# Kernel tuning notes

Measured on AMD Instinct MI355X. Metric: run time of the kernel, lower is better.

The kernel has to match this reference:

```python
import jax, jax.numpy as jnp
import numpy as np
from jax import lax

HEADS = 8
DIM_HEAD = 8
SCALE = DIM_HEAD ** (-0.5)
UP = 64  # nn.Upsample(scale_factor=64), nearest


def _conv_s8(x, w, b):
    # Conv2d(inner, inner, 11x11, stride 8, padding 2) + exact GELU
    y = lax.conv_general_dilated(x, w, window_strides=(8, 8),
                                 padding=((2, 2), (2, 2)),
                                 dimension_numbers=('NCHW', 'OIHW', 'NCHW'))
    return jax.nn.gelu(y + b[None, :, None, None], approximate=False)


def setup_inputs() -> dict:
    key = jax.random.key(0)
    ks = jax.random.split(key, 8)
    b, c, h, w = 2, 64, 48, 48
    inner = HEADS * DIM_HEAD  # 64
    f = jax.random.normal(ks[0], (b, c, h, w), jnp.float32)
    w_qkv = jax.random.normal(ks[1], (inner * 3, c, 1, 1), jnp.float32) * 0.05
    wq = jax.random.normal(ks[2], (inner, inner, 11, 11), jnp.float32) * 0.02
    bq = jax.random.normal(ks[3], (inner,), jnp.float32) * 0.02
    wk = jax.random.normal(ks[4], (inner, inner, 11, 11), jnp.float32) * 0.02
    bk = jax.random.normal(ks[5], (inner,), jnp.float32) * 0.02
    pos_h = jax.random.normal(ks[6], (DIM_HEAD, h), jnp.float32) * SCALE
    pos_w = jax.random.normal(ks[7], (DIM_HEAD, w), jnp.float32) * SCALE
    return {"f": f, "w_qkv": w_qkv, "wq": wq, "bq": bq, "wk": wk,
            "bk": bk, "pos_h": pos_h, "pos_w": pos_w}


def reference(f, w_qkv, wq, bq, wk, bk, pos_h, pos_w):
    b, c, h, w = f.shape
    inner = HEADS * DIM_HEAD
    # 1x1 conv to qkv
    qkv = jnp.einsum('oc,bchw->bohw', w_qkv[:, :, 0, 0], f)
    q, k, v = jnp.split(qkv, 3, axis=1)  # each [b, inner, h, w]
    # positional logits from pre-conv q
    q_full = q.reshape(b, HEADS, DIM_HEAD, h * w)
    emb = (pos_h[:, :, None] + pos_w[:, None, :]).reshape(DIM_HEAD, h * w)
    pos_logits = jnp.einsum('bhci,cj->bhij', q_full, emb)  # [b,H,hw,hw]
    # strided conv + gelu on q,k
    qd = _conv_s8(q, wq, bq)
    kd = _conv_s8(k, wk, bk)
    m = qd.shape[-1]  # downsampled side
    qd = qd.reshape(b, HEADS, DIM_HEAD, m * m) * SCALE
    kd = kd.reshape(b, HEADS, DIM_HEAD, m * m)
    vv = v.reshape(b, HEADS, DIM_HEAD, h * w)
    dots = jnp.einsum('bhci,bhcj->bhij', qd, kd)  # [b,H,m^2,m^2]
    # nearest upsample x64 on last two dims
    dots = jnp.repeat(jnp.repeat(dots, UP, axis=-2), UP, axis=-1)
    attn = jax.nn.softmax(dots + pos_logits, axis=-1)
    fmap = jnp.einsum('bhij,bhcj->bhci', attn, vv)
    return fmap.reshape(b, inner, h, w)
```

## Files before the change

### kernel.cpp

```cpp
#include <hip/hip_runtime.h>
#include <math.h>

#define HW 2304
#define O192 192
#define SCALE_F 0.35355339059327373f

typedef unsigned int u32;
typedef __attribute__((address_space(1))) const u32 gu32;
typedef __attribute__((address_space(3))) u32 lu32;
__device__ __forceinline__ void dma16(const void* g, void* l) {
  __builtin_amdgcn_global_load_lds((gu32*)g, (lu32*)l, 16, 0, 0);
}

__global__ __launch_bounds__(256) void qkv_kernel(
    const float* __restrict__ F, const float* __restrict__ W,
    float* __restrict__ QKV, float* __restrict__ V2) {
  __shared__ __align__(16) float sW[384];
  int blk = blockIdx.x;
  int idx0 = blk * 256;
  int r0 = idx0 / HW;
  int r1 = (idx0 + 255) / HW;
  int tid = threadIdx.x;
  if (tid < 192) {
    int g = tid >> 6, c = tid & 63;
    sW[tid]       = W[((r0 & 63) + g * 64) * 64 + c];
    sW[192 + tid] = W[((r1 & 63) + g * 64) * 64 + c];
  }
  __syncthreads();
  int idx = idx0 + tid;
  int p  = idx % HW;
  int r  = idx / HW;
  int o0 = r & 63;
  int b  = r >> 6;
  const float4* w4 = (const float4*)(sW + ((r == r0) ? 0 : 192));
  const float* f = F + (b * 64) * HW + p;
  float aq = 0.f, ak = 0.f, av = 0.f;
  #pragma unroll 4
  for (int c4 = 0; c4 < 16; c4++) {
    float4 wq = w4[c4];
    float4 wk = w4[16 + c4];
    float4 wv = w4[32 + c4];
    float f0 = f[(c4 * 4 + 0) * HW];
    float f1 = f[(c4 * 4 + 1) * HW];
    float f2 = f[(c4 * 4 + 2) * HW];
    float f3 = f[(c4 * 4 + 3) * HW];
    aq = fmaf(wq.x, f0, aq); ak = fmaf(wk.x, f0, ak); av = fmaf(wv.x, f0, av);
    aq = fmaf(wq.y, f1, aq); ak = fmaf(wk.y, f1, ak); av = fmaf(wv.y, f1, av);
    aq = fmaf(wq.z, f2, aq); ak = fmaf(wk.z, f2, ak); av = fmaf(wv.z, f2, av);
    aq = fmaf(wq.w, f3, aq); ak = fmaf(wk.w, f3, ak); av = fmaf(wv.w, f3, av);
  }
  float* qp = QKV + (b * HW + p) * O192;
  qp[o0]      = aq;
  qp[o0 + 64] = ak;
  V2[(((b << 3) + (o0 >> 3)) * HW + p) * 8 + (o0 & 7)] = av;
}

__global__ __launch_bounds__(256) void conv_kernel(
    const float* __restrict__ QKV, const float* __restrict__ Wq,
    const float* __restrict__ Bq, const float* __restrict__ Wk,
    const float* __restrict__ Bk, float* __restrict__ QD) {
  __shared__ float sW[7744];
  __shared__ float sRed[4 * 64 * 6];
  int blk = blockIdx.x;
  int xcd = blk & 7;
  int T = xcd >> 2, b = (xcd >> 1) & 1, s = xcd & 1;
  int idx = (blk >> 3) * 2 + s;
  int o  = idx / 6;
  int oy = idx % 6;
  const float* Wg = T ? Wk : Wq;
  for (int i = threadIdx.x; i < 7744; i += 256) sW[i] = Wg[o * 7744 + i];
  __syncthreads();
  int wv = threadIdx.x >> 6;
  int c  = threadIdx.x & 63;
  const float* base = QKV + b * (HW * O192) + T * 64 + c;
  float acc[6];
  #pragma unroll
  for (int ox = 0; ox < 6; ox++) acc[ox] = 0.f;
  for (int kyi = 0; kyi < 3; kyi++) {
    int ky = wv * 3 + kyi;
    if (ky > 10) break;
    int y = oy * 8 - 2 + ky;
    if ((unsigned)y < 48u) {
      float xrow[48];
      #pragma unroll
      for (int x = 0; x < 48; x++) xrow[x] = base[(y * 48 + x) * O192];
      #pragma unroll
      for (int kx = 0; kx < 11; kx++) {
        float wt = sW[c * 121 + ky * 11 + kx];
        #pragma unroll
        for (int ox = 0; ox < 6; ox++) {
          int x = ox * 8 - 2 + kx;
          if (x >= 0 && x < 48) acc[ox] = fmaf(xrow[x], wt, acc[ox]);
        }
      }
    }
  }
  #pragma unroll
  for (int ox = 0; ox < 6; ox++) sRed[(wv * 64 + c) * 6 + ox] = acc[ox];
  __syncthreads();
  if (threadIdx.x < 64) {
    int t = threadIdx.x;
    float r[6];
    #pragma unroll
    for (int ox = 0; ox < 6; ox++)
      r[ox] = sRed[t * 6 + ox] + sRed[(64 + t) * 6 + ox]
            + sRed[(128 + t) * 6 + ox] + sRed[(192 + t) * 6 + ox];
    #pragma unroll
    for (int off = 32; off; off >>= 1) {
      #pragma unroll
      for (int ox = 0; ox < 6; ox++) r[ox] += __shfl_down(r[ox], off, 64);
    }
    if (t == 0) {
      float bias = T ? Bk[o] : Bq[o];
      #pragma unroll
      for (int ox = 0; ox < 6; ox++) {
        float g = r[ox] + bias;
        float ge = 0.5f * g * (1.0f + erff(g * 0.70710678118654752f));
        QD[((T * 2 + b) * 64 + o) * 36 + oy * 6 + ox] = ge;
      }
    }
  }
}

#define OFF_V    0
#define OFF_QLO  4608
#define OFF_QHI  5120
#define OFF_EA   5632
#define OFF_PHT  11776
#define OFF_PWT  12160
#define OFF_E    12544
#define OFF_Z    12616
#define SBUF_N   12648

__global__ __launch_bounds__(512) void attn_kernel(
    const float* __restrict__ QKV, const float* __restrict__ V2,
    const float* __restrict__ QD, const float* __restrict__ PH,
    const float* __restrict__ PW, float* __restrict__ out) {
  __shared__ __align__(16) float sB[SBUF_N];
  int blk = blockIdx.x;
  int bh = blk & 15;
  int Ip = blk >> 4;
  int b = bh >> 3, h = bh & 7;
  int r0 = Ip * 128;
  int tid = threadIdx.x;
  int w = tid >> 6, lane = tid & 63;
  int l32 = lane & 31, chalf = lane >> 5;
  if (tid < 384) {
    sB[OFF_PHT + tid] = PH[(tid & 7) * 48 + (tid >> 3)];
    sB[OFF_PWT + tid] = PW[(tid & 7) * 48 + (tid >> 3)];
  }
  if (tid < 72) {
    int Ik = tid / 36, J = tid - Ik * 36;
    const float* qd = QD + ((0 + b) * 64 + h * 8) * 36 + (Ip * 2 + Ik);
    const float* kd = QD + ((2 + b) * 64 + h * 8) * 36 + J;
    float acc = 0.f;
    #pragma unroll
    for (int c8 = 0; c8 < 8; c8++) acc = fmaf(qd[c8 * 36], kd[c8 * 36], acc);
    sB[OFF_E + tid] = __expf(SCALE_F * acc);
  }
  if (tid < 256) {
    int row = tid >> 1, half = tid & 1;
    int slot = (row & 31) * 4 + (row >> 5);
    float4 qv = *(const float4*)(QKV + (b * HW + r0 + row) * O192 + h * 8 + half * 4);
    *(float4*)(sB + (half ? OFF_QHI : OFF_QLO) + slot * 4) = qv;
  }
  __syncthreads();
  #pragma unroll
  for (int m = 0; m < 12; m++) {
    int flat = tid + m * 512;
    int jy = flat >> 7, s = flat & 127;
    float4 qa = *(const float4*)(sB + OFF_QLO + s * 4);
    float4 qb = *(const float4*)(sB + OFF_QHI + s * 4);
    const float* pp = sB + OFF_PHT + jy * 8;
    float d = qa.x*pp[0]+qa.y*pp[1]+qa.z*pp[2]+qa.w*pp[3]
            + qb.x*pp[4]+qb.y*pp[5]+qb.z*pp[6]+qb.w*pp[7];
    sB[OFF_EA + flat] = __expf(d);
  }
  float eB[4][6];
  #pragma unroll
  for (int k8 = 0; k8 < 4; k8++) {
    float4 qa = *(const float4*)(sB + OFF_QLO + (l32 * 4 + k8) * 4);
    float4 qb = *(const float4*)(sB + OFF_QHI + (l32 * 4 + k8) * 4);
    #pragma unroll
    for (int i = 0; i < 6; i++) {
      const float* pp = sB + OFF_PWT + (w * 6 + i) * 8;
      float d = qa.x*pp[0]+qa.y*pp[1]+qa.z*pp[2]+qa.w*pp[3]
              + qb.x*pp[4]+qb.y*pp[5]+qb.z*pp[6]+qb.w*pp[7];
      eB[k8][i] = __expf(d);
    }
  }
  float accv[4][4], zz[4];
  #pragma unroll
  for (int k8 = 0; k8 < 4; k8++) {
    zz[k8] = 0.f;
    #pragma unroll
    for (int c = 0; c < 4; c++) accv[k8][c] = 0.f;
  }
  const float4* sV4 = (const float4*)(sB + OFF_V);
  for (int p = 0; p < 4; p++) {
    __syncthreads();
    {
      const char* src = (const char*)(V2 + (size_t)bh * (HW * 8) + p * 4608);
      for (int m = w; m < 18; m += 8)
        dma16(src + m * 1024 + lane * 16, (char*)(sB + OFF_V) + m * 1024);
    }
    __syncthreads();
    #pragma unroll
    for (int jyL = 0; jyL < 12; jyL++) {
      int jy = p * 12 + jyL;
      float4 ea = *(const float4*)(sB + OFF_EA + jy * 128 + l32 * 4);
      int cb = jy * 48 + w * 6;
      int J0 = cb >> 6, J1 = (cb + 5) >> 6;
      int ib = 64 - (cb & 63);
      float e00 = sB[OFF_E + J0], e01 = sB[OFF_E + 36 + J0];
      float e10 = sB[OFF_E + J1], e11 = sB[OFF_E + 36 + J1];
      float a0[4], a1[4];
      a0[0] = ea.x * e00; a0[1] = ea.y * e00;
      a0[2] = ea.z * e01; a0[3] = ea.w * e01;
      a1[0] = ea.x * e10; a1[1] = ea.y * e10;
      a1[2] = ea.z * e11; a1[3] = ea.w * e11;
      #pragma unroll
      for (int i = 0; i < 6; i++) {
        float4 v = sV4[(jyL * 48 + w * 6 + i) * 2 + chalf];
        bool s0 = (i < ib);
        #pragma unroll
        for (int k8 = 0; k8 < 4; k8++) {
          float wgt = (s0 ? a0[k8] : a1[k8]) * eB[k8][i];
          accv[k8][0] = fmaf(wgt, v.x, accv[k8][0]);
          accv[k8][1] = fmaf(wgt, v.y, accv[k8][1]);
          accv[k8][2] = fmaf(wgt, v.z, accv[k8][2]);
          accv[k8][3] = fmaf(wgt, v.w, accv[k8][3]);
          zz[k8] += wgt;
        }
      }
    }
  }
  float* sU = sB + OFF_EA;
  #pragma unroll
  for (int k8 = 0; k8 < 4; k8++) {
    __syncthreads();
    {
      float* rp = sU + (w * 64 + lane) * 5;
      rp[0] = accv[k8][0]; rp[1] = accv[k8][1];
      rp[2] = accv[k8][2]; rp[3] = accv[k8][3];
      rp[4] = zz[k8];
    }
    __syncthreads();
    if (tid < 32) {
      float z = 0.f;
      #pragma unroll
      for (int ww = 0; ww < 8; ww++)
        z += sU[(ww * 64 + tid) * 5 + 4] + sU[(ww * 64 + 32 + tid) * 5 + 4];
      sB[OFF_Z + tid] = 2.0f / z;
    }
    __syncthreads();
    if (tid < 256) {
      int row32 = tid & 31, c = tid >> 5;
      int ln = ((c >> 2) << 5) + row32;
      float num = 0.f;
      #pragma unroll
      for (int ww = 0; ww < 8; ww++) num += sU[(ww * 64 + ln) * 5 + (c & 3)];
      out[(b * 64 + h * 8 + c) * HW + r0 + k8 * 32 + row32] =
          num * sB[OFF_Z + row32];
    }
  }
}

extern "C" void kernel_launch(void* const* d_in, const int* in_sizes, int n_in,
                              void* d_out, int out_size, void* d_ws, size_t ws_size,
                              hipStream_t stream) {
  const float* F    = (const float*)d_in[0];
  const float* Wqkv = (const float*)d_in[1];
  const float* Wq   = (const float*)d_in[2];
  const float* Bq   = (const float*)d_in[3];
  const float* Wk   = (const float*)d_in[4];
  const float* Bk   = (const float*)d_in[5];
  const float* PH   = (const float*)d_in[6];
  const float* PW   = (const float*)d_in[7];
  float* out = (float*)d_out;

  float* ws  = (float*)d_ws;
  float* QKV = ws;
  float* V2  = QKV + 2 * HW * O192;
  float* QD  = V2 + 2 * 8 * HW * 8;

  qkv_kernel <<<1152, 256, 0, stream>>>(F, Wqkv, QKV, V2);
  conv_kernel<<<1536, 256, 0, stream>>>(QKV, Wq, Bq, Wk, Bk, QD);
  attn_kernel<<<288,  512, 0, stream>>>(QKV, V2, QD, PH, PW, out);
}
```

Measured before the change: 159.6 us.

## Split attention key range across two blocks and combine partials in new kernel

The attention kernel now splits the key rows (jy) into two halves, so each block processes 24 of the 48 key rows and the grid doubles from 288 to 576 blocks. Each block writes unnormalized numerators and partial softmax denominators to workspace, and a new combine kernel sums the two halves and divides. This is meant to fill more compute units on the MI355X, since 288 blocks underfill the device. In exchange it adds an extra kernel launch and a round trip of the partials through global memory.

```diff
diff --git a/kernel.cpp b/kernel.cpp
--- a/kernel.cpp
+++ b/kernel.cpp
@@ -126,28 +126,36 @@
 #define OFF_QLO  4608
 #define OFF_QHI  5120
 #define OFF_EA   5632
-#define OFF_PHT  11776
-#define OFF_PWT  12160
-#define OFF_E    12544
-#define OFF_Z    12616
-#define SBUF_N   12648
+#define OFF_PHT  8704
+#define OFF_PWT  8896
+#define OFF_E    9280
+#define OFF_Z    9352
+#define SBUF_N   9384
 
 __global__ __launch_bounds__(512) void attn_kernel(
     const float* __restrict__ QKV, const float* __restrict__ V2,
     const float* __restrict__ QD, const float* __restrict__ PH,
-    const float* __restrict__ PW, float* __restrict__ out) {
+    const float* __restrict__ PW, float* __restrict__ Pnum,
+    float* __restrict__ PZ) {
   __shared__ __align__(16) float sB[SBUF_N];
   int blk = blockIdx.x;
   int bh = blk & 15;
-  int Ip = blk >> 4;
+  int jh = (blk >> 4) & 1;
+  int Ip = blk >> 5;
   int b = bh >> 3, h = bh & 7;
   int r0 = Ip * 128;
   int tid = threadIdx.x;
   int w = tid >> 6, lane = tid & 63;
   int l32 = lane & 31, chalf = lane >> 5;
-  if (tid < 384) {
-    sB[OFF_PHT + tid] = PH[(tid & 7) * 48 + (tid >> 3)];
-    sB[OFF_PWT + tid] = PW[(tid & 7) * 48 + (tid >> 3)];
+  if (tid < 192) {
+    sB[OFF_PHT + tid] = PH[(tid & 7) * 48 + jh * 24 + (tid >> 3)];
+  } else {
+    int i = tid - 192;
+    sB[OFF_PWT + i] = PW[(i & 7) * 48 + (i >> 3)];
+  }
+  if (tid < 64) {
+    int i = 320 + tid;
+    sB[OFF_PWT + i] = PW[(i & 7) * 48 + (i >> 3)];
   }
   if (tid < 72) {
     int Ik = tid / 36, J = tid - Ik * 36;
@@ -166,12 +174,12 @@
   }
   __syncthreads();
   #pragma unroll
-  for (int m = 0; m < 12; m++) {
+  for (int m = 0; m < 6; m++) {
     int flat = tid + m * 512;
-    int jy = flat >> 7, s = flat & 127;
+    int jyRel = flat >> 7, s = flat & 127;
     float4 qa = *(const float4*)(sB + OFF_QLO + s * 4);
     float4 qb = *(const float4*)(sB + OFF_QHI + s * 4);
-    const float* pp = sB + OFF_PHT + jy * 8;
+    const float* pp = sB + OFF_PHT + jyRel * 8;
     float d = qa.x*pp[0]+qa.y*pp[1]+qa.z*pp[2]+qa.w*pp[3]
             + qb.x*pp[4]+qb.y*pp[5]+qb.z*pp[6]+qb.w*pp[7];
     sB[OFF_EA + flat] = __expf(d);
@@ -197,18 +205,20 @@
     for (int c = 0; c < 4; c++) accv[k8][c] = 0.f;
   }
   const float4* sV4 = (const float4*)(sB + OFF_V);
-  for (int p = 0; p < 4; p++) {
+  for (int p = 0; p < 2; p++) {
+    int pq = jh * 2 + p;
     __syncthreads();
     {
-      const char* src = (const char*)(V2 + (size_t)bh * (HW * 8) + p * 4608);
+      const char* src = (const char*)(V2 + (size_t)bh * (HW * 8) + pq * 4608);
       for (int m = w; m < 18; m += 8)
         dma16(src + m * 1024 + lane * 16, (char*)(sB + OFF_V) + m * 1024);
     }
     __syncthreads();
     #pragma unroll
     for (int jyL = 0; jyL < 12; jyL++) {
-      int jy = p * 12 + jyL;
-      float4 ea = *(const float4*)(sB + OFF_EA + jy * 128 + l32 * 4);
+      int jyRel = p * 12 + jyL;
+      int jy = jh * 24 + jyRel;
+      float4 ea = *(const float4*)(sB + OFF_EA + jyRel * 128 + l32 * 4);
       int cb = jy * 48 + w * 6;
       int J0 = cb >> 6, J1 = (cb + 5) >> 6;
       int ib = 64 - (cb & 63);
@@ -246,24 +256,36 @@
       rp[4] = zz[k8];
     }
     __syncthreads();
-    if (tid < 32) {
-      float z = 0.f;
-      #pragma unroll
-      for (int ww = 0; ww < 8; ww++)
-        z += sU[(ww * 64 + tid) * 5 + 4] + sU[(ww * 64 + 32 + tid) * 5 + 4];
-      sB[OFF_Z + tid] = 2.0f / z;
-    }
-    __syncthreads();
     if (tid < 256) {
       int row32 = tid & 31, c = tid >> 5;
       int ln = ((c >> 2) << 5) + row32;
       float num = 0.f;
       #pragma unroll
       for (int ww = 0; ww < 8; ww++) num += sU[(ww * 64 + ln) * 5 + (c & 3)];
-      out[(b * 64 + h * 8 + c) * HW + r0 + k8 * 32 + row32] =
-          num * sB[OFF_Z + row32];
-    }
-  }
+      Pnum[((jh * 16 + bh) * 8 + c) * HW + r0 + k8 * 32 + row32] = num;
+    } else if (tid < 288) {
+      int row32 = tid & 31;
+      float z = 0.f;
+      #pragma unroll
+      for (int ww = 0; ww < 8; ww++)
+        z += sU[(ww * 64 + row32) * 5 + 4] + sU[(ww * 64 + 32 + row32) * 5 + 4];
+      PZ[(jh * 16 + bh) * HW + r0 + k8 * 32 + row32] = z * 0.5f;
+    }
+  }
+}
+
+__global__ __launch_bounds__(256) void combine_kernel(
+    const float* __restrict__ Pnum, const float* __restrict__ PZ,
+    float* __restrict__ out) {
+  int t = blockIdx.x * 256 + threadIdx.x;
+  int row = t % HW;
+  int rc = t / HW;
+  int c = rc & 7, bh = rc >> 3;
+  float num = Pnum[((bh) * 8 + c) * HW + row]
+            + Pnum[((16 + bh) * 8 + c) * HW + row];
+  float z = PZ[bh * HW + row] + PZ[(16 + bh) * HW + row];
+  int b = bh >> 3, h = bh & 7;
+  out[(b * 64 + h * 8 + c) * HW + row] = num / z;
 }
 
 extern "C" void kernel_launch(void* const* d_in, const int* in_sizes, int n_in,
@@ -279,12 +301,15 @@
   const float* PW   = (const float*)d_in[7];
   float* out = (float*)d_out;
 
-  float* ws  = (float*)d_ws;
-  float* QKV = ws;
-  float* V2  = QKV + 2 * HW * O192;
-  float* QD  = V2 + 2 * 8 * HW * 8;
-
-  qkv_kernel <<<1152, 256, 0, stream>>>(F, Wqkv, QKV, V2);
-  conv_kernel<<<1536, 256, 0, stream>>>(QKV, Wq, Bq, Wk, Bk, QD);
-  attn_kernel<<<288,  512, 0, stream>>>(QKV, V2, QD, PH, PW, out);
-}
+  float* ws   = (float*)d_ws;
+  float* QKV  = ws;
+  float* V2   = QKV + 2 * HW * O192;
+  float* QD   = V2 + 2 * 8 * HW * 8;
+  float* Pnum = QD + 2 * 2 * 64 * 36;
+  float* PZ   = Pnum + 2 * 16 * 8 * HW;
+
+  qkv_kernel    <<<1152, 256, 0, stream>>>(F, Wqkv, QKV, V2);
+  conv_kernel   <<<1536, 256, 0, stream>>>(QKV, Wq, Bq, Wk, Bk, QD);
+  attn_kernel   <<<576,  512, 0, stream>>>(QKV, V2, QD, PH, PW, Pnum, PZ);
+  combine_kernel<<<1152, 256, 0, stream>>>(Pnum, PZ, out);
+}
```

Result: faster. 153.8 us (-3.6%).
